# Kernel optimization log

Measured on AMD Instinct MI355X. Metric: run time of the kernel, lower is better.

## Reference

```python
import jax, jax.numpy as jnp
import numpy as np

B, S, D = 8, 2048, 1024

def setup_inputs() -> dict:
    key = jax.random.key(0)
    ks = jax.random.split(key, 9)
    s = 1.0 / np.sqrt(D)
    return {
        "x": jax.random.normal(ks[0], (B, S, D), dtype=jnp.float32),
        "Wq": jax.random.uniform(ks[1], (D, D), jnp.float32, -s, s),
        "bq": jax.random.uniform(ks[2], (D,), jnp.float32, -s, s),
        "Wk": jax.random.uniform(ks[3], (D, D), jnp.float32, -s, s),
        "bk": jax.random.uniform(ks[4], (D,), jnp.float32, -s, s),
        "Wv": jax.random.uniform(ks[5], (D, D), jnp.float32, -s, s),
        "bv": jax.random.uniform(ks[6], (D,), jnp.float32, -s, s),
        "Wo": jax.random.uniform(ks[7], (D, 1), jnp.float32, -s, s),
        "bo": jax.random.uniform(ks[8], (1,), jnp.float32, -s, s),
    }

def reference(x, Wq, bq, Wk, bk, Wv, bv, Wo, bo):
    q = x @ Wq + bq                      # [B,S,D]
    k = x @ Wk + bk                      # [B,S,D]
    v = x @ Wv + bv                      # [B,S,D]
    scores = jnp.einsum('bsd,btd->bst', q, k)   # [B,S,S], NOTE: no 1/sqrt(D) scaling in source
    attn = jax.nn.softmax(scores, axis=-1)
    out = jnp.einsum('bst,btd->bsd', attn, v)   # [B,S,D]
    return out @ Wo + bo                 # [B,S,1]
```

## Files before the change

kernel.cpp:

```cpp
#include <hip/hip_runtime.h>
#include <stdint.h>

#define D_ 1024
#define S_ 2048
#define B_ 8

typedef _Float16 h16;
typedef _Float16 f16x8 __attribute__((ext_vector_type(8)));
typedef _Float16 f16x4 __attribute__((ext_vector_type(4)));
typedef float    f32x4 __attribute__((ext_vector_type(4)));

typedef __attribute__((address_space(3))) void lds_void;
typedef const __attribute__((address_space(1))) void g_void;

#define MFMA16(a, b, c) __builtin_amdgcn_mfma_f32_16x16x32_f16(a, b, c, 0, 0, 0)
#define VMCNT(n) asm volatile("s_waitcnt vmcnt(" #n ")" ::: "memory")
#define SFENCE() __builtin_amdgcn_sched_barrier(0)
#define SBAR() __builtin_amdgcn_s_barrier()

__device__ __forceinline__ void stage16(const h16* g0, int ld, h16* lchunk) {
  int lane = threadIdx.x & 63;
  int c = (lane & 3) ^ ((lane >> 3) & 3);
  const h16* ga = g0 + (size_t)(lane >> 2) * ld + c * 8;
  __builtin_amdgcn_global_load_lds((g_void*)ga, (lds_void*)lchunk, 16, 0, 0);
}

__global__ void k_u(const float* __restrict__ Wv, const float* __restrict__ Wo,
                    const float* __restrict__ bv, float* __restrict__ u) {
  int lane = threadIdx.x & 63;
  if (blockIdx.x == 256) {
    if (threadIdx.x < 64) {
      float s = 0.f;
      #pragma unroll
      for (int j = 0; j < 4; ++j) {
        float4 a = ((const float4*)bv)[j * 64 + lane];
        float4 b = ((const float4*)Wo)[j * 64 + lane];
        s += a.x * b.x + a.y * b.y + a.z * b.z + a.w * b.w;
      }
      #pragma unroll
      for (int off = 32; off; off >>= 1) s += __shfl_xor(s, off, 64);
      if (lane == 0) u[D_] = s;
    }
    return;
  }
  int row = blockIdx.x * 4 + (threadIdx.x >> 6);
  const float4* r4 = (const float4*)(Wv + (size_t)row * D_);
  const float4* w4 = (const float4*)Wo;
  float s = 0.f;
  #pragma unroll
  for (int j = 0; j < 4; ++j) {
    int c = j * 64 + lane;
    float4 a = r4[c], b = w4[c];
    s += a.x * b.x + a.y * b.y + a.z * b.z + a.w * b.w;
  }
  #pragma unroll
  for (int off = 32; off; off >>= 1) s += __shfl_xor(s, off, 64);
  if (lane == 0) u[row] = s;
}

__global__ void k_wt(const float* __restrict__ Wq, const float* __restrict__ Wk,
                     h16* __restrict__ Wt) {
  __shared__ float t[32][33];
  int n0 = blockIdx.x * 32;
  int k0 = blockIdx.y * 32;
  const float* src = (n0 < D_) ? Wq : Wk;
  int nn = n0 & (D_ - 1);
  int tx = threadIdx.x, ty = threadIdx.y;
  for (int i = ty; i < 32; i += 8)
    t[i][tx] = src[(size_t)(k0 + i) * D_ + nn + tx];
  __syncthreads();
  for (int i = ty; i < 32; i += 8)
    Wt[(size_t)(n0 + i) * D_ + k0 + tx] = (h16)t[tx][i];
}

__global__ void k_xw(const float* __restrict__ x, const float* __restrict__ u,
                     h16* __restrict__ xh, float* __restrict__ w) {
  int row = blockIdx.x * 4 + (threadIdx.x >> 6);
  int lane = threadIdx.x & 63;
  const float4* xr = (const float4*)(x + (size_t)row * D_);
  const float4* u4 = (const float4*)u;
  h16* xo = xh + (size_t)row * D_;
  float s = 0.f;
  #pragma unroll
  for (int j = 0; j < 4; ++j) {
    int c = j * 64 + lane;
    float4 a = xr[c];
    float4 b = u4[c];
    s += a.x * b.x + a.y * b.y + a.z * b.z + a.w * b.w;
    f16x4 o;
    o[0] = (h16)a.x; o[1] = (h16)a.y; o[2] = (h16)a.z; o[3] = (h16)a.w;
    *(f16x4*)(xo + c * 4) = o;
  }
  #pragma unroll
  for (int off = 32; off; off >>= 1) s += __shfl_xor(s, off, 64);
  if (lane == 0) w[row] = s + u[D_];
}

__global__ __launch_bounds__(512, 4) void k_proj(
    const h16* __restrict__ xh, const h16* __restrict__ Wt,
    const float* __restrict__ bq_, const float* __restrict__ bk_,
    h16* __restrict__ qkh) {
  __shared__ alignas(16) h16 As[3][256 * 32];
  __shared__ alignas(16) h16 Bs[3][128 * 32];
  int tid = threadIdx.x;
  int w = tid >> 6;
  int lane = tid & 63;
  int wrow = w >> 1, wcol = w & 1;
  int g = lane >> 4, l15 = lane & 15;
  int swz = (l15 >> 1) & 3;

  int idx = (blockIdx.x & 7) * 128 + (blockIdx.x >> 3);
  int m0 = (idx >> 4) * 256, n0 = (idx & 15) * 128;

  const h16* abase0 = xh + (size_t)(m0 + (2 * w) * 16) * D_;
  const h16* abase1 = abase0 + (size_t)16 * D_;
  const h16* bbase  = Wt + (size_t)(n0 + w * 16) * D_;

  f32x4 acc[4][4] = {};

  #define STAGE_PROJ(ap, bp, k)                              \
    {                                                        \
      int k0_ = (k) * 32;                                    \
      stage16(abase0 + k0_, D_, (ap) + (2 * w) * 512);       \
      stage16(abase1 + k0_, D_, (ap) + (2 * w + 1) * 512);   \
      stage16(bbase + k0_, D_, (bp) + w * 512);              \
    }

  h16 *A0 = As[0], *A1 = As[1], *A2 = As[2];
  h16 *B0 = Bs[0], *B1 = Bs[1], *B2 = Bs[2];
  STAGE_PROJ(A0, B0, 0);
  STAGE_PROJ(A1, B1, 1);
  for (int k = 0; k < 32; ++k) {
    if (k + 2 < 32) {
      STAGE_PROJ(A2, B2, k + 2);
      VMCNT(6);
    } else if (k + 1 < 32) {
      VMCNT(3);
    } else {
      VMCNT(0);
    }
    SFENCE();
    SBAR();
    SFENCE();
    f16x8 af[4], bf[4];
    #pragma unroll
    for (int i = 0; i < 4; ++i) {
      af[i] = *(const f16x8*)(A0 + (wrow * 64 + i * 16 + l15) * 32 + (g ^ swz) * 8);
      bf[i] = *(const f16x8*)(B0 + (wcol * 64 + i * 16 + l15) * 32 + (g ^ swz) * 8);
    }
    __builtin_amdgcn_s_setprio(1);
    #pragma unroll
    for (int mi = 0; mi < 4; ++mi)
      #pragma unroll
      for (int ni = 0; ni < 4; ++ni)
        acc[mi][ni] = MFMA16(af[mi], bf[ni], acc[mi][ni]);
    __builtin_amdgcn_s_setprio(0);
    SBAR();
    h16* t;
    t = A0; A0 = A1; A1 = A2; A2 = t;
    t = B0; B0 = B1; B1 = B2; B2 = t;
  }

  #pragma unroll
  for (int ni = 0; ni < 4; ++ni) {
    int n = n0 + wcol * 64 + ni * 16 + l15;
    float bias = (n < D_) ? bq_[n] : bk_[n - D_];
    #pragma unroll
    for (int mi = 0; mi < 4; ++mi) {
      #pragma unroll
      for (int r = 0; r < 4; ++r) {
        int m = m0 + wrow * 64 + mi * 16 + g * 4 + r;
        qkh[(size_t)m * (2 * D_) + n] = (h16)(acc[mi][ni][r] + bias);
      }
    }
  }
}

__global__ __launch_bounds__(512, 4) void k_attn(
    const h16* __restrict__ qkh, const float* __restrict__ wv,
    float* __restrict__ part) {
  __shared__ alignas(16) h16 Qs[3][128 * 32];
  __shared__ alignas(16) h16 Ks[3][256 * 32];
  __shared__ float sm[3][4][128];
  int tid = threadIdx.x;
  int w = tid >> 6;
  int lane = tid & 63;
  int g = lane >> 4, l15 = lane & 15;
  int swz = (l15 >> 1) & 3;
  int wq = w >> 2, wkc = w & 3;
  int b = blockIdx.x & 7;
  int r = blockIdx.x >> 3;
  int kc = r >> 4;
  int q0 = (r & 15) * 128;
  size_t rbase = (size_t)b * S_;

  const h16* qbase  = qkh + (rbase + q0 + w * 16) * (2 * D_);
  const h16* kbase0 = qkh + (rbase + kc * 256 + (2 * w) * 16) * (2 * D_) + D_;
  const h16* kbase1 = kbase0 + (size_t)16 * (2 * D_);

  #define STAGE_ATTN(qp, kp, st)                             \
    {                                                        \
      int k0_ = (st) * 32;                                   \
      stage16(qbase + k0_, 2 * D_, (qp) + w * 512);          \
      stage16(kbase0 + k0_, 2 * D_, (kp) + (2 * w) * 512);   \
      stage16(kbase1 + k0_, 2 * D_, (kp) + (2 * w + 1) * 512); \
    }

  f32x4 acc[4][4] = {};

  h16 *Q0 = Qs[0], *Q1 = Qs[1], *Q2 = Qs[2];
  h16 *K0 = Ks[0], *K1 = Ks[1], *K2 = Ks[2];
  STAGE_ATTN(Q0, K0, 0);
  STAGE_ATTN(Q1, K1, 1);
  for (int st = 0; st < 32; ++st) {
    if (st + 2 < 32) {
      STAGE_ATTN(Q2, K2, st + 2);
      VMCNT(6);
    } else if (st + 1 < 32) {
      VMCNT(3);
    } else {
      VMCNT(0);
    }
    SFENCE();
    SBAR();
    SFENCE();
    f16x8 qf[4], kf[4];
    #pragma unroll
    for (int i = 0; i < 4; ++i) {
      qf[i] = *(const f16x8*)(Q0 + (wq * 64 + i * 16 + l15) * 32 + (g ^ swz) * 8);
      kf[i] = *(const f16x8*)(K0 + (wkc * 64 + i * 16 + l15) * 32 + (g ^ swz) * 8);
    }
    __builtin_amdgcn_s_setprio(1);
    #pragma unroll
    for (int mi = 0; mi < 4; ++mi)
      #pragma unroll
      for (int ni = 0; ni < 4; ++ni)
        acc[mi][ni] = MFMA16(qf[mi], kf[ni], acc[mi][ni]);
    __builtin_amdgcn_s_setprio(0);
    SBAR();
    h16* t;
    t = Q0; Q0 = Q1; Q1 = Q2; Q2 = t;
    t = K0; K0 = K1; K1 = K2; K2 = t;
  }

  float wvv[4];
  #pragma unroll
  for (int ni = 0; ni < 4; ++ni)
    wvv[ni] = wv[rbase + kc * 256 + wkc * 64 + ni * 16 + l15];
  #pragma unroll
  for (int mi = 0; mi < 4; ++mi) {
    #pragma unroll
    for (int rr = 0; rr < 4; ++rr) {
      float v = fmaxf(fmaxf(acc[mi][0][rr], acc[mi][1][rr]),
                      fmaxf(acc[mi][2][rr], acc[mi][3][rr]));
      #pragma unroll
      for (int off = 1; off < 16; off <<= 1) v = fmaxf(v, __shfl_xor(v, off, 64));
      float pn = 0.f, pd = 0.f;
      #pragma unroll
      for (int ni = 0; ni < 4; ++ni) {
        float p = __expf(acc[mi][ni][rr] - v);
        pn += p * wvv[ni];
        pd += p;
      }
      #pragma unroll
      for (int off = 1; off < 16; off <<= 1) {
        pn += __shfl_xor(pn, off, 64);
        pd += __shfl_xor(pd, off, 64);
      }
      if (l15 == 0) {
        int row = wq * 64 + mi * 16 + g * 4 + rr;
        sm[0][wkc][row] = v;
        sm[1][wkc][row] = pn;
        sm[2][wkc][row] = pd;
      }
    }
  }
  __syncthreads();
  if (tid < 128) {
    float M = sm[0][0][tid];
    #pragma unroll
    for (int j = 1; j < 4; ++j) M = fmaxf(M, sm[0][j][tid]);
    float N = 0.f, Dn = 0.f;
    #pragma unroll
    for (int j = 0; j < 4; ++j) {
      float e = __expf(sm[0][j][tid] - M);
      N += sm[1][j][tid] * e;
      Dn += sm[2][j][tid] * e;
    }
    size_t row = rbase + q0 + tid;
    part[row * 24 + kc * 3 + 0] = M;
    part[row * 24 + kc * 3 + 1] = N;
    part[row * 24 + kc * 3 + 2] = Dn;
  }
}

__global__ void k_fin(const float* __restrict__ part, const float* __restrict__ bo,
                      float* __restrict__ out) {
  int idx = blockIdx.x * 256 + threadIdx.x;
  if (idx >= B_ * S_) return;
  const float* p = part + (size_t)idx * 24;
  float M = p[0];
  #pragma unroll
  for (int j = 1; j < 8; ++j) M = fmaxf(M, p[j * 3]);
  float N = 0.f, Dn = 0.f;
  #pragma unroll
  for (int j = 0; j < 8; ++j) {
    float e = __expf(p[j * 3] - M);
    N += p[j * 3 + 1] * e;
    Dn += p[j * 3 + 2] * e;
  }
  out[idx] = N / Dn + bo[0];
}

extern "C" void kernel_launch(void* const* d_in, const int* in_sizes, int n_in,
                              void* d_out, int out_size, void* d_ws, size_t ws_size,
                              hipStream_t stream) {
  const float* x  = (const float*)d_in[0];
  const float* Wq = (const float*)d_in[1];
  const float* bq = (const float*)d_in[2];
  const float* Wk = (const float*)d_in[3];
  const float* bk = (const float*)d_in[4];
  const float* Wv = (const float*)d_in[5];
  const float* bv = (const float*)d_in[6];
  const float* Wo = (const float*)d_in[7];
  const float* bo = (const float*)d_in[8];
  float* out = (float*)d_out;

  char* ws = (char*)d_ws;
  h16*   xh   = (h16*)ws;
  h16*   Wt   = (h16*)(ws + (size_t)32 * 1024 * 1024);
  h16*   qkh  = (h16*)(ws + (size_t)36 * 1024 * 1024);
  float* wv   = (float*)(ws + (size_t)100 * 1024 * 1024);
  float* u    = (float*)(ws + (size_t)100 * 1024 * 1024 + 65536);
  float* part = (float*)(ws + (size_t)101 * 1024 * 1024);

  hipLaunchKernelGGL(k_u,    dim3(257),    dim3(256),   0, stream, Wv, Wo, bv, u);
  hipLaunchKernelGGL(k_wt,   dim3(64, 32), dim3(32, 8), 0, stream, Wq, Wk, Wt);
  hipLaunchKernelGGL(k_xw,   dim3(4096),   dim3(256),   0, stream, x, u, xh, wv);
  hipLaunchKernelGGL(k_proj, dim3(1024),   dim3(512),   0, stream, xh, Wt, bq, bk, qkh);
  hipLaunchKernelGGL(k_attn, dim3(1024),   dim3(512),   0, stream, qkh, wv, part);
  hipLaunchKernelGGL(k_fin,  dim3(64),     dim3(256),   0, stream, part, bo, out);
}
```

Measured before the change: 280.1 us.

## Fold Wq·Wkᵀ into one matrix so attention scores use x directly as keys

Rewrites the scores as (x·Wq·Wkᵀ)·xᵀ plus a per-key bias term x·Wk·bq, so the key projection disappears. Terms that are constant along each softmax row (bk contributions) are dropped because softmax is invariant to them. The Q/K projection GEMM (N=2048) becomes a small 1024³ weight product plus an N=1024 GEMM, roughly halving projection FLOPs and the qkh traffic. The cost is an extra fp16 rounding of the fused M matrix, which may hurt accuracy because the scores are unscaled and large.

```diff
diff --git a/kernel.cpp b/kernel.cpp
--- a/kernel.cpp
+++ b/kernel.cpp
@@ -25,8 +25,24 @@
   __builtin_amdgcn_global_load_lds((g_void*)ga, (lds_void*)lchunk, 16, 0, 0);
 }
 
-__global__ void k_u(const float* __restrict__ Wv, const float* __restrict__ Wo,
-                    const float* __restrict__ bv, float* __restrict__ u) {
+__global__ void k_cast(const float* __restrict__ Wq, const float* __restrict__ Wk,
+                       h16* __restrict__ Wqh, h16* __restrict__ Wkh) {
+  int i = blockIdx.x * 256 + threadIdx.x;
+  const int n4 = (D_ * D_) / 4;
+  const float4* src;
+  h16* dst;
+  if (i < n4) { src = (const float4*)Wq; dst = Wqh; }
+  else        { src = (const float4*)Wk; dst = Wkh; i -= n4; }
+  float4 a = src[i];
+  f16x4 o;
+  o[0] = (h16)a.x; o[1] = (h16)a.y; o[2] = (h16)a.z; o[3] = (h16)a.w;
+  *(f16x4*)(dst + (size_t)i * 4) = o;
+}
+
+__global__ void k_u(const float* __restrict__ Wv, const float* __restrict__ Wk,
+                    const float* __restrict__ Wo, const float* __restrict__ bq_,
+                    const float* __restrict__ bv, float* __restrict__ u,
+                    float* __restrict__ v2) {
   int lane = threadIdx.x & 63;
   if (blockIdx.x == 256) {
     if (threadIdx.x < 64) {
@@ -44,81 +60,155 @@
     return;
   }
   int row = blockIdx.x * 4 + (threadIdx.x >> 6);
-  const float4* r4 = (const float4*)(Wv + (size_t)row * D_);
+  const float4* rv = (const float4*)(Wv + (size_t)row * D_);
+  const float4* rk = (const float4*)(Wk + (size_t)row * D_);
   const float4* w4 = (const float4*)Wo;
-  float s = 0.f;
+  const float4* b4 = (const float4*)bq_;
+  float s1 = 0.f, s2 = 0.f;
   #pragma unroll
   for (int j = 0; j < 4; ++j) {
     int c = j * 64 + lane;
-    float4 a = r4[c], b = w4[c];
-    s += a.x * b.x + a.y * b.y + a.z * b.z + a.w * b.w;
-  }
-  #pragma unroll
-  for (int off = 32; off; off >>= 1) s += __shfl_xor(s, off, 64);
-  if (lane == 0) u[row] = s;
-}
-
-__global__ void k_wt(const float* __restrict__ Wq, const float* __restrict__ Wk,
-                     h16* __restrict__ Wt) {
-  __shared__ float t[32][33];
-  int n0 = blockIdx.x * 32;
-  int k0 = blockIdx.y * 32;
-  const float* src = (n0 < D_) ? Wq : Wk;
-  int nn = n0 & (D_ - 1);
-  int tx = threadIdx.x, ty = threadIdx.y;
-  for (int i = ty; i < 32; i += 8)
-    t[i][tx] = src[(size_t)(k0 + i) * D_ + nn + tx];
-  __syncthreads();
-  for (int i = ty; i < 32; i += 8)
-    Wt[(size_t)(n0 + i) * D_ + k0 + tx] = (h16)t[tx][i];
+    float4 a = rv[c], b = w4[c];
+    s1 += a.x * b.x + a.y * b.y + a.z * b.z + a.w * b.w;
+    float4 e = rk[c], f = b4[c];
+    s2 += e.x * f.x + e.y * f.y + e.z * f.z + e.w * f.w;
+  }
+  #pragma unroll
+  for (int off = 32; off; off >>= 1) {
+    s1 += __shfl_xor(s1, off, 64);
+    s2 += __shfl_xor(s2, off, 64);
+  }
+  if (lane == 0) { u[row] = s1; v2[row] = s2; }
 }
 
 __global__ void k_xw(const float* __restrict__ x, const float* __restrict__ u,
-                     h16* __restrict__ xh, float* __restrict__ w) {
+                     const float* __restrict__ v2, h16* __restrict__ xh,
+                     float* __restrict__ w, float* __restrict__ cv) {
   int row = blockIdx.x * 4 + (threadIdx.x >> 6);
   int lane = threadIdx.x & 63;
   const float4* xr = (const float4*)(x + (size_t)row * D_);
   const float4* u4 = (const float4*)u;
+  const float4* c4 = (const float4*)v2;
   h16* xo = xh + (size_t)row * D_;
-  float s = 0.f;
+  float s1 = 0.f, s2 = 0.f;
   #pragma unroll
   for (int j = 0; j < 4; ++j) {
     int c = j * 64 + lane;
     float4 a = xr[c];
     float4 b = u4[c];
-    s += a.x * b.x + a.y * b.y + a.z * b.z + a.w * b.w;
+    float4 e = c4[c];
+    s1 += a.x * b.x + a.y * b.y + a.z * b.z + a.w * b.w;
+    s2 += a.x * e.x + a.y * e.y + a.z * e.z + a.w * e.w;
     f16x4 o;
     o[0] = (h16)a.x; o[1] = (h16)a.y; o[2] = (h16)a.z; o[3] = (h16)a.w;
     *(f16x4*)(xo + c * 4) = o;
   }
   #pragma unroll
-  for (int off = 32; off; off >>= 1) s += __shfl_xor(s, off, 64);
-  if (lane == 0) w[row] = s + u[D_];
-}
-
-__global__ __launch_bounds__(512, 4) void k_proj(
-    const h16* __restrict__ xh, const h16* __restrict__ Wt,
-    const float* __restrict__ bq_, const float* __restrict__ bk_,
-    h16* __restrict__ qkh) {
+  for (int off = 32; off; off >>= 1) {
+    s1 += __shfl_xor(s1, off, 64);
+    s2 += __shfl_xor(s2, off, 64);
+  }
+  if (lane == 0) { w[row] = s1 + u[D_]; cv[row] = s2; }
+}
+
+__global__ __launch_bounds__(256, 4) void k_mt(
+    const h16* __restrict__ Wkh, const h16* __restrict__ Wqh,
+    h16* __restrict__ Mt) {
+  __shared__ alignas(16) h16 As[3][128 * 32];
+  __shared__ alignas(16) h16 Bs[3][128 * 32];
+  int tid = threadIdx.x;
+  int w = tid >> 6, lane = tid & 63;
+  int wr = w >> 1, wc = w & 1;
+  int g = lane >> 4, l15 = lane & 15;
+  int swz = (l15 >> 1) & 3;
+  int m0 = (blockIdx.x >> 3) * 128, n0 = (blockIdx.x & 7) * 128;
+
+  const h16* abase0 = Wkh + (size_t)(m0 + (2 * w) * 16) * D_;
+  const h16* abase1 = abase0 + (size_t)16 * D_;
+  const h16* bbase0 = Wqh + (size_t)(n0 + (2 * w) * 16) * D_;
+  const h16* bbase1 = bbase0 + (size_t)16 * D_;
+
+  f32x4 acc[4][4] = {};
+
+  #define STAGE_MT(ap, bp, k)                                \
+    {                                                        \
+      int k0_ = (k) * 32;                                    \
+      stage16(abase0 + k0_, D_, (ap) + (2 * w) * 512);       \
+      stage16(abase1 + k0_, D_, (ap) + (2 * w + 1) * 512);   \
+      stage16(bbase0 + k0_, D_, (bp) + (2 * w) * 512);       \
+      stage16(bbase1 + k0_, D_, (bp) + (2 * w + 1) * 512);   \
+    }
+
+  h16 *A0 = As[0], *A1 = As[1], *A2 = As[2];
+  h16 *B0 = Bs[0], *B1 = Bs[1], *B2 = Bs[2];
+  STAGE_MT(A0, B0, 0);
+  STAGE_MT(A1, B1, 1);
+  for (int k = 0; k < 32; ++k) {
+    if (k + 2 < 32) {
+      STAGE_MT(A2, B2, k + 2);
+      VMCNT(8);
+    } else if (k + 1 < 32) {
+      VMCNT(4);
+    } else {
+      VMCNT(0);
+    }
+    SFENCE();
+    SBAR();
+    SFENCE();
+    f16x8 af[4], bf[4];
+    #pragma unroll
+    for (int i = 0; i < 4; ++i) {
+      af[i] = *(const f16x8*)(A0 + (wr * 64 + i * 16 + l15) * 32 + (g ^ swz) * 8);
+      bf[i] = *(const f16x8*)(B0 + (wc * 64 + i * 16 + l15) * 32 + (g ^ swz) * 8);
+    }
+    __builtin_amdgcn_s_setprio(1);
+    #pragma unroll
+    for (int mi = 0; mi < 4; ++mi)
+      #pragma unroll
+      for (int ni = 0; ni < 4; ++ni)
+        acc[mi][ni] = MFMA16(af[mi], bf[ni], acc[mi][ni]);
+    __builtin_amdgcn_s_setprio(0);
+    SBAR();
+    h16* t;
+    t = A0; A0 = A1; A1 = A2; A2 = t;
+    t = B0; B0 = B1; B1 = B2; B2 = t;
+  }
+
+  #pragma unroll
+  for (int ni = 0; ni < 4; ++ni) {
+    int n = n0 + wc * 64 + ni * 16 + l15;
+    #pragma unroll
+    for (int mi = 0; mi < 4; ++mi) {
+      #pragma unroll
+      for (int r = 0; r < 4; ++r) {
+        int m = m0 + wr * 64 + mi * 16 + g * 4 + r;
+        Mt[(size_t)m * D_ + n] = (h16)(acc[mi][ni][r]);
+      }
+    }
+  }
+}
+
+__global__ __launch_bounds__(512, 4) void k_y(
+    const h16* __restrict__ xh, const h16* __restrict__ Mt,
+    h16* __restrict__ y) {
   __shared__ alignas(16) h16 As[3][256 * 32];
   __shared__ alignas(16) h16 Bs[3][128 * 32];
   int tid = threadIdx.x;
-  int w = tid >> 6;
-  int lane = tid & 63;
+  int w = tid >> 6, lane = tid & 63;
   int wrow = w >> 1, wcol = w & 1;
   int g = lane >> 4, l15 = lane & 15;
   int swz = (l15 >> 1) & 3;
 
-  int idx = (blockIdx.x & 7) * 128 + (blockIdx.x >> 3);
-  int m0 = (idx >> 4) * 256, n0 = (idx & 15) * 128;
+  int idx = (blockIdx.x & 7) * 64 + (blockIdx.x >> 3);
+  int m0 = (idx >> 3) * 256, n0 = (idx & 7) * 128;
 
   const h16* abase0 = xh + (size_t)(m0 + (2 * w) * 16) * D_;
   const h16* abase1 = abase0 + (size_t)16 * D_;
-  const h16* bbase  = Wt + (size_t)(n0 + w * 16) * D_;
+  const h16* bbase  = Mt + (size_t)(n0 + w * 16) * D_;
 
   f32x4 acc[4][4] = {};
 
-  #define STAGE_PROJ(ap, bp, k)                              \
+  #define STAGE_Y(ap, bp, k)                                 \
     {                                                        \
       int k0_ = (k) * 32;                                    \
       stage16(abase0 + k0_, D_, (ap) + (2 * w) * 512);       \
@@ -128,11 +218,11 @@
 
   h16 *A0 = As[0], *A1 = As[1], *A2 = As[2];
   h16 *B0 = Bs[0], *B1 = Bs[1], *B2 = Bs[2];
-  STAGE_PROJ(A0, B0, 0);
-  STAGE_PROJ(A1, B1, 1);
+  STAGE_Y(A0, B0, 0);
+  STAGE_Y(A1, B1, 1);
   for (int k = 0; k < 32; ++k) {
     if (k + 2 < 32) {
-      STAGE_PROJ(A2, B2, k + 2);
+      STAGE_Y(A2, B2, k + 2);
       VMCNT(6);
     } else if (k + 1 < 32) {
       VMCNT(3);
@@ -164,27 +254,26 @@
   #pragma unroll
   for (int ni = 0; ni < 4; ++ni) {
     int n = n0 + wcol * 64 + ni * 16 + l15;
-    float bias = (n < D_) ? bq_[n] : bk_[n - D_];
     #pragma unroll
     for (int mi = 0; mi < 4; ++mi) {
       #pragma unroll
       for (int r = 0; r < 4; ++r) {
         int m = m0 + wrow * 64 + mi * 16 + g * 4 + r;
-        qkh[(size_t)m * (2 * D_) + n] = (h16)(acc[mi][ni][r] + bias);
+        y[(size_t)m * D_ + n] = (h16)(acc[mi][ni][r]);
       }
     }
   }
 }
 
 __global__ __launch_bounds__(512, 4) void k_attn(
-    const h16* __restrict__ qkh, const float* __restrict__ wv,
+    const h16* __restrict__ y, const h16* __restrict__ xh,
+    const float* __restrict__ wv, const float* __restrict__ cv,
     float* __restrict__ part) {
   __shared__ alignas(16) h16 Qs[3][128 * 32];
   __shared__ alignas(16) h16 Ks[3][256 * 32];
   __shared__ float sm[3][4][128];
   int tid = threadIdx.x;
-  int w = tid >> 6;
-  int lane = tid & 63;
+  int w = tid >> 6, lane = tid & 63;
   int g = lane >> 4, l15 = lane & 15;
   int swz = (l15 >> 1) & 3;
   int wq = w >> 2, wkc = w & 3;
@@ -194,16 +283,16 @@
   int q0 = (r & 15) * 128;
   size_t rbase = (size_t)b * S_;
 
-  const h16* qbase  = qkh + (rbase + q0 + w * 16) * (2 * D_);
-  const h16* kbase0 = qkh + (rbase + kc * 256 + (2 * w) * 16) * (2 * D_) + D_;
-  const h16* kbase1 = kbase0 + (size_t)16 * (2 * D_);
+  const h16* qbase  = y + (rbase + q0 + w * 16) * D_;
+  const h16* kbase0 = xh + (rbase + kc * 256 + (2 * w) * 16) * D_;
+  const h16* kbase1 = kbase0 + (size_t)16 * D_;
 
   #define STAGE_ATTN(qp, kp, st)                             \
     {                                                        \
       int k0_ = (st) * 32;                                   \
-      stage16(qbase + k0_, 2 * D_, (qp) + w * 512);          \
-      stage16(kbase0 + k0_, 2 * D_, (kp) + (2 * w) * 512);   \
-      stage16(kbase1 + k0_, 2 * D_, (kp) + (2 * w + 1) * 512); \
+      stage16(qbase + k0_, D_, (qp) + w * 512);              \
+      stage16(kbase0 + k0_, D_, (kp) + (2 * w) * 512);       \
+      stage16(kbase1 + k0_, D_, (kp) + (2 * w + 1) * 512);   \
     }
 
   f32x4 acc[4][4] = {};
@@ -243,25 +332,28 @@
     t = K0; K0 = K1; K1 = K2; K2 = t;
   }
 
-  float wvv[4];
-  #pragma unroll
-  for (int ni = 0; ni < 4; ++ni)
-    wvv[ni] = wv[rbase + kc * 256 + wkc * 64 + ni * 16 + l15];
+  float wvv[4], cvv[4];
+  #pragma unroll
+  for (int ni = 0; ni < 4; ++ni) {
+    size_t t = rbase + kc * 256 + wkc * 64 + ni * 16 + l15;
+    wvv[ni] = wv[t];
+    cvv[ni] = cv[t];
+  }
   #pragma unroll
   for (int mi = 0; mi < 4; ++mi) {
     #pragma unroll
     for (int rr = 0; rr < 4; ++rr) {
-      float v = fmaxf(fmaxf(acc[mi][0][rr], acc[mi][1][rr]),
-                      fmaxf(acc[mi][2][rr], acc[mi][3][rr]));
+      float s0 = acc[mi][0][rr] + cvv[0];
+      float s1 = acc[mi][1][rr] + cvv[1];
+      float s2 = acc[mi][2][rr] + cvv[2];
+      float s3 = acc[mi][3][rr] + cvv[3];
+      float v = fmaxf(fmaxf(s0, s1), fmaxf(s2, s3));
       #pragma unroll
       for (int off = 1; off < 16; off <<= 1) v = fmaxf(v, __shfl_xor(v, off, 64));
-      float pn = 0.f, pd = 0.f;
-      #pragma unroll
-      for (int ni = 0; ni < 4; ++ni) {
-        float p = __expf(acc[mi][ni][rr] - v);
-        pn += p * wvv[ni];
-        pd += p;
-      }
+      float p0 = __expf(s0 - v), p1 = __expf(s1 - v);
+      float p2 = __expf(s2 - v), p3 = __expf(s3 - v);
+      float pn = p0 * wvv[0] + p1 * wvv[1] + p2 * wvv[2] + p3 * wvv[3];
+      float pd = p0 + p1 + p2 + p3;
       #pragma unroll
       for (int off = 1; off < 16; off <<= 1) {
         pn += __shfl_xor(pn, off, 64);
@@ -325,19 +417,25 @@
   const float* Wo = (const float*)d_in[7];
   const float* bo = (const float*)d_in[8];
   float* out = (float*)d_out;
+  (void)bk;
 
   char* ws = (char*)d_ws;
   h16*   xh   = (h16*)ws;
-  h16*   Wt   = (h16*)(ws + (size_t)32 * 1024 * 1024);
-  h16*   qkh  = (h16*)(ws + (size_t)36 * 1024 * 1024);
-  float* wv   = (float*)(ws + (size_t)100 * 1024 * 1024);
-  float* u    = (float*)(ws + (size_t)100 * 1024 * 1024 + 65536);
-  float* part = (float*)(ws + (size_t)101 * 1024 * 1024);
-
-  hipLaunchKernelGGL(k_u,    dim3(257),    dim3(256),   0, stream, Wv, Wo, bv, u);
-  hipLaunchKernelGGL(k_wt,   dim3(64, 32), dim3(32, 8), 0, stream, Wq, Wk, Wt);
-  hipLaunchKernelGGL(k_xw,   dim3(4096),   dim3(256),   0, stream, x, u, xh, wv);
-  hipLaunchKernelGGL(k_proj, dim3(1024),   dim3(512),   0, stream, xh, Wt, bq, bk, qkh);
-  hipLaunchKernelGGL(k_attn, dim3(1024),   dim3(512),   0, stream, qkh, wv, part);
-  hipLaunchKernelGGL(k_fin,  dim3(64),     dim3(256),   0, stream, part, bo, out);
-}
+  h16*   yb   = (h16*)(ws + (size_t)32 * 1024 * 1024);
+  h16*   Mt   = (h16*)(ws + (size_t)64 * 1024 * 1024);
+  h16*   Wqh  = (h16*)(ws + (size_t)66 * 1024 * 1024);
+  h16*   Wkh  = (h16*)(ws + (size_t)68 * 1024 * 1024);
+  float* wv   = (float*)(ws + (size_t)70 * 1024 * 1024);
+  float* cv   = (float*)(ws + (size_t)70 * 1024 * 1024 + 65536);
+  float* u    = (float*)(ws + (size_t)70 * 1024 * 1024 + 131072);
+  float* v2   = (float*)(ws + (size_t)70 * 1024 * 1024 + 139264);
+  float* part = (float*)(ws + (size_t)71 * 1024 * 1024);
+
+  hipLaunchKernelGGL(k_cast, dim3(2048), dim3(256), 0, stream, Wq, Wk, Wqh, Wkh);
+  hipLaunchKernelGGL(k_u,    dim3(257),  dim3(256), 0, stream, Wv, Wk, Wo, bq, bv, u, v2);
+  hipLaunchKernelGGL(k_xw,   dim3(4096), dim3(256), 0, stream, x, u, v2, xh, wv, cv);
+  hipLaunchKernelGGL(k_mt,   dim3(64),   dim3(256), 0, stream, Wkh, Wqh, Mt);
+  hipLaunchKernelGGL(k_y,    dim3(512),  dim3(512), 0, stream, xh, Mt, yb);
+  hipLaunchKernelGGL(k_attn, dim3(1024), dim3(512), 0, stream, yb, xh, wv, cv, part);
+  hipLaunchKernelGGL(k_fin,  dim3(64),   dim3(256), 0, stream, part, bo, out);
+}
```

After: 269.0 us. 1.04x faster.
